# Kernel tuning notes

Hardware: AMD Instinct MI355X
Metric: run time of the kernel (lower is better)

The kernel has to match this reference:

```python
import jax, jax.numpy as jnp
import numpy as np

N = 50000          # nodes in homogeneous graph
E_RAND = 450000    # non-self edges
R = 5              # 4 relations + identity
C = 2              # num_channels
L = 2              # num_layers
IN_DIM = 256
HID = 128
NUM_CLASS = 16
N_CAT = 10000


def setup_inputs() -> dict:
    key = jax.random.key(0)
    ks = jax.random.split(key, 10)
    h = jax.random.normal(ks[0], (N, IN_DIM), dtype=jnp.float32)
    src_r = jax.random.randint(ks[1], (E_RAND,), 0, N, dtype=jnp.int32)
    dst_r = jax.random.randint(ks[2], (E_RAND,), 0, N, dtype=jnp.int32)
    et_r = jax.random.randint(ks[3], (E_RAND,), 0, R - 1, dtype=jnp.int32)
    self_idx = jnp.arange(N, dtype=jnp.int32)
    src = jnp.concatenate([src_r, self_idx])
    dst = jnp.concatenate([dst_r, self_idx])
    etype = jnp.concatenate([et_r, jnp.full((N,), R - 1, dtype=jnp.int32)])
    category_idx = jax.random.randint(ks[4], (N_CAT,), 0, N, dtype=jnp.int32)
    # learned params
    gt_w = 0.01 * jax.random.normal(ks[5], (L, C, R), dtype=jnp.float32)
    Wc = jax.random.normal(ks[6], (C, IN_DIM, HID), dtype=jnp.float32) / np.sqrt(IN_DIM)
    W1 = jax.random.normal(ks[7], (C * HID, HID), dtype=jnp.float32) / np.sqrt(C * HID)
    b1 = jnp.zeros((HID,), dtype=jnp.float32)
    W2 = jax.random.normal(ks[8], (HID, NUM_CLASS), dtype=jnp.float32) / np.sqrt(HID)
    b2 = jnp.zeros((NUM_CLASS,), dtype=jnp.float32)
    return {"h": h, "src": src, "dst": dst, "etype": etype,
            "category_idx": category_idx, "gt_w": gt_w, "Wc": Wc,
            "W1": W1, "b1": b1, "W2": W2, "b2": b2}


def reference(h, src, dst, etype, category_idx, gt_w, Wc, W1, b1, W2, b2):
    n = h.shape[0]
    # per-channel input projection: H[c] = h @ Wc[c]  -> [C, N, HID]
    H = jnp.einsum('nd,cdh->cnh', h, Wc)
    seg = lambda v: jax.ops.segment_sum(v, dst, num_segments=n)
    for l in range(gt_w.shape[0]):
        # GTConv: per-channel softmax over relations; summed weighted adjacency
        Filt = jax.nn.softmax(gt_w[l], axis=1)        # [C, R]
        w = Filt[:, etype]                            # [C, E] edge weights
        # EdgeWeightNorm('right'): divide by weighted in-degree of dst
        deg = jax.vmap(seg)(w)                        # [C, N]
        wn = w / deg[:, dst]                          # [C, E]
        # GCNConv: sum_{e: dst=v} H[src(e)] * wn(e)
        msg = H[:, src, :] * wn[:, :, None]           # [C, E, HID]
        H = jax.vmap(seg)(msg)                        # [C, N, HID]
    # concat channels along feature dim (torch.cat(H, dim=1))
    X = jnp.transpose(H, (1, 0, 2)).reshape(n, -1)    # [N, C*HID]
    X = jax.nn.relu(X @ W1 + b1)
    y = X @ W2 + b2
    return y[category_idx]
```

## Files before the change

### kernel.cpp

```cpp
#include <hip/hip_runtime.h>
#include <hip/hip_bf16.h>

#define IN_DIM 256
#define HID 128
#define CCH 2
#define RR 5
#define LL 2
#define NCLS 16

typedef __attribute__((ext_vector_type(8))) short short8;
typedef __attribute__((ext_vector_type(4))) short short4_;
typedef __attribute__((ext_vector_type(4))) float floatx4;

__device__ __forceinline__ unsigned short f2bf(float f) {
    unsigned int u = __float_as_uint(f);
    unsigned int r = (u + 0x7FFFu + ((u >> 16) & 1u)) >> 16;
    return (unsigned short)r;
}

__global__ void cvt_weights(const float* __restrict__ Wc, const float* __restrict__ W1,
                            const float* __restrict__ gt_w,
                            unsigned short* __restrict__ WcT, unsigned short* __restrict__ W1T,
                            float* __restrict__ filt) {
    int i = blockIdx.x * 256 + threadIdx.x;
    if (blockIdx.x == 0 && threadIdx.x < LL * CCH) {
        const float* g = gt_w + threadIdx.x * RR;
        float m = -1e30f;
        for (int r = 0; r < RR; ++r) m = fmaxf(m, g[r]);
        float e[RR], s = 0.f;
        for (int r = 0; r < RR; ++r) { e[r] = __expf(g[r] - m); s += e[r]; }
        for (int r = 0; r < RR; ++r) filt[threadIdx.x * RR + r] = e[r] / s;
    }
    if (i < CCH * HID * IN_DIM) {
        int c = i >> 15;
        int rem = i & 32767;
        int d = rem >> 8;
        int k = rem & 255;
        WcT[i] = f2bf(Wc[((size_t)c * IN_DIM + k) * HID + d]);
    }
    if (i < HID * IN_DIM) {
        int d = i >> 8;
        int k = i & 255;
        W1T[i] = f2bf(W1[(size_t)k * HID + d]);
    }
}

__global__ __launch_bounds__(256) void proj_mfma(const float* __restrict__ h,
                                                 const unsigned short* __restrict__ WcT,
                                                 unsigned short* __restrict__ H0, int N) {
    int t = threadIdx.x;
    int wv = t >> 6, l = t & 63;
    int l15 = l & 15, lq = l >> 4;
    int node = blockIdx.x * 64 + wv * 16 + l15;
    int nclamp = node < N ? node : N - 1;

    short8 bfrag[8];
    const float* hrow = h + (size_t)nclamp * IN_DIM;
#pragma unroll
    for (int kk = 0; kk < 8; ++kk) {
        int k0 = kk * 32 + lq * 8;
        floatx4 f0 = *(const floatx4*)(hrow + k0);
        floatx4 f1 = *(const floatx4*)(hrow + k0 + 4);
        short8 b;
        b[0] = (short)f2bf(f0[0]); b[1] = (short)f2bf(f0[1]);
        b[2] = (short)f2bf(f0[2]); b[3] = (short)f2bf(f0[3]);
        b[4] = (short)f2bf(f1[0]); b[5] = (short)f2bf(f1[1]);
        b[6] = (short)f2bf(f1[2]); b[7] = (short)f2bf(f1[3]);
        bfrag[kk] = b;
    }

#pragma unroll
    for (int mt = 0; mt < 16; ++mt) {
        floatx4 acc = {0.f, 0.f, 0.f, 0.f};
        const unsigned short* arow = WcT + (size_t)(mt * 16 + l15) * IN_DIM;
#pragma unroll
        for (int kk = 0; kk < 8; ++kk) {
            short8 a = *(const short8*)(arow + kk * 32 + lq * 8);
            acc = __builtin_amdgcn_mfma_f32_16x16x32_bf16(a, bfrag[kk], acc, 0, 0, 0);
        }
        if (node < N) {
            int m0 = mt * 16 + lq * 4;
            short4_ st;
            st[0] = (short)f2bf(acc[0]); st[1] = (short)f2bf(acc[1]);
            st[2] = (short)f2bf(acc[2]); st[3] = (short)f2bf(acc[3]);
            *(short4_*)(H0 + (size_t)node * (CCH * HID) + m0) = st;
        }
    }
}

__global__ void count_kernel(const int* __restrict__ dst, int* __restrict__ counts, int E) {
    for (int e = blockIdx.x * blockDim.x + threadIdx.x; e < E; e += gridDim.x * blockDim.x)
        atomicAdd(&counts[dst[e]], 1);
}

__global__ void scanA_kernel(const int* __restrict__ counts, int* __restrict__ partials, int n) {
    __shared__ int s[256];
    int t = threadIdx.x;
    int i = blockIdx.x * 256 + t;
    int v = (i < n) ? counts[i] : 0;
    s[t] = v;
    __syncthreads();
    for (int off = 1; off < 256; off <<= 1) {
        int tv = (t >= off) ? s[t - off] : 0;
        __syncthreads();
        s[t] += tv;
        __syncthreads();
    }
    if (t == 255) partials[blockIdx.x] = s[255];
}

__global__ void scanB_kernel(const int* __restrict__ partials, int* __restrict__ chunk_off, int nchunk) {
    __shared__ int s[256];
    int t = threadIdx.x;
    int v = (t < nchunk) ? partials[t] : 0;
    s[t] = v;
    __syncthreads();
    for (int off = 1; off < 256; off <<= 1) {
        int tv = (t >= off) ? s[t - off] : 0;
        __syncthreads();
        s[t] += tv;
        __syncthreads();
    }
    if (t < nchunk) chunk_off[t] = s[t] - v;
}

__global__ void scanC_kernel(const int* __restrict__ counts, const int* __restrict__ chunk_off,
                             int* __restrict__ offsets, int* __restrict__ cursor, int n) {
    __shared__ int s[256];
    int t = threadIdx.x;
    int i = blockIdx.x * 256 + t;
    int v = (i < n) ? counts[i] : 0;
    s[t] = v;
    __syncthreads();
    for (int off = 1; off < 256; off <<= 1) {
        int tv = (t >= off) ? s[t - off] : 0;
        __syncthreads();
        s[t] += tv;
        __syncthreads();
    }
    if (i < n) {
        int incl = chunk_off[blockIdx.x] + s[t];
        offsets[i + 1] = incl;
        cursor[i] = incl - v;
    }
    if (i == 0) offsets[0] = 0;
}

__global__ void fill_kernel(const int* __restrict__ src, const int* __restrict__ dst,
                            const int* __restrict__ etype, int* __restrict__ cursor,
                            int2* __restrict__ epack, int E) {
    for (int e = blockIdx.x * blockDim.x + threadIdx.x; e < E; e += gridDim.x * blockDim.x) {
        int d = dst[e];
        int p = atomicAdd(&cursor[d], 1);
        epack[p] = make_int2(src[e], etype[e]);
    }
}

__global__ __launch_bounds__(256) void agg_kernel(const uint4* __restrict__ Hin,
                                                  uint4* __restrict__ Hout,
                                                  const int* __restrict__ offs,
                                                  const int2* __restrict__ epack,
                                                  const float* __restrict__ filt, int N) {
    int node = blockIdx.x;
    int t = threadIdx.x;
    int g = t >> 5;
    int lane32 = t & 31;
    int c = lane32 >> 4;
    float f0 = filt[c * RR + 0], f1 = filt[c * RR + 1], f2 = filt[c * RR + 2];
    float f3 = filt[c * RR + 3], f4 = filt[c * RR + 4];

    int e0 = offs[node], e1 = offs[node + 1];
    float acc[8];
#pragma unroll
    for (int r = 0; r < 8; ++r) acc[r] = 0.f;
    float deg = 0.f;

    for (int j = e0 + g; j < e1; j += 8) {
        int2 pc = epack[j];
        uint4 v = Hin[(size_t)pc.x * 32 + lane32];
        int et = pc.y;
        float w = (et == 0) ? f0 : (et == 1) ? f1 : (et == 2) ? f2 : (et == 3) ? f3 : f4;
        deg += w;
        acc[0] += w * __uint_as_float(v.x << 16);
        acc[1] += w * __uint_as_float(v.x & 0xFFFF0000u);
        acc[2] += w * __uint_as_float(v.y << 16);
        acc[3] += w * __uint_as_float(v.y & 0xFFFF0000u);
        acc[4] += w * __uint_as_float(v.z << 16);
        acc[5] += w * __uint_as_float(v.z & 0xFFFF0000u);
        acc[6] += w * __uint_as_float(v.w << 16);
        acc[7] += w * __uint_as_float(v.w & 0xFFFF0000u);
    }

#pragma unroll
    for (int r = 0; r < 8; ++r) acc[r] += __shfl_xor(acc[r], 32);
    deg += __shfl_xor(deg, 32);

    __shared__ float sacc[3][8][33];
    __shared__ float sdeg[3][33];
    int wv = t >> 6;
    bool lowhalf = (t & 63) < 32;
    if (wv > 0 && lowhalf) {
#pragma unroll
        for (int r = 0; r < 8; ++r) sacc[wv - 1][r][lane32] = acc[r];
        sdeg[wv - 1][lane32] = deg;
    }
    __syncthreads();
    if (wv == 0 && lowhalf) {
#pragma unroll
        for (int k = 0; k < 3; ++k) {
#pragma unroll
            for (int r = 0; r < 8; ++r) acc[r] += sacc[k][r][lane32];
            deg += sdeg[k][lane32];
        }
        float inv = 1.f / deg;
        uint4 o;
        o.x = (unsigned int)f2bf(acc[0] * inv) | ((unsigned int)f2bf(acc[1] * inv) << 16);
        o.y = (unsigned int)f2bf(acc[2] * inv) | ((unsigned int)f2bf(acc[3] * inv) << 16);
        o.z = (unsigned int)f2bf(acc[4] * inv) | ((unsigned int)f2bf(acc[5] * inv) << 16);
        o.w = (unsigned int)f2bf(acc[6] * inv) | ((unsigned int)f2bf(acc[7] * inv) << 16);
        Hout[(size_t)node * 32 + lane32] = o;
    }
}

__global__ __launch_bounds__(256) void mlp1_mfma(const unsigned short* __restrict__ H2,
                                                 const int* __restrict__ cat,
                                                 const unsigned short* __restrict__ W1T,
                                                 const float* __restrict__ b1,
                                                 float* __restrict__ hidden, int NCAT) {
    int t = threadIdx.x;
    int wv = t >> 6, l = t & 63;
    int l15 = l & 15, lq = l >> 4;
    int i = blockIdx.x * 64 + wv * 16 + l15;
    int iclamp = i < NCAT ? i : NCAT - 1;
    int node = cat[iclamp];

    short8 bfrag[8];
    const unsigned short* xrow = H2 + (size_t)node * (CCH * HID);
#pragma unroll
    for (int kk = 0; kk < 8; ++kk)
        bfrag[kk] = *(const short8*)(xrow + kk * 32 + lq * 8);

#pragma unroll
    for (int mt = 0; mt < 8; ++mt) {
        floatx4 acc = {0.f, 0.f, 0.f, 0.f};
        const unsigned short* arow = W1T + (size_t)(mt * 16 + l15) * (CCH * HID);
#pragma unroll
        for (int kk = 0; kk < 8; ++kk) {
            short8 a = *(const short8*)(arow + kk * 32 + lq * 8);
            acc = __builtin_amdgcn_mfma_f32_16x16x32_bf16(a, bfrag[kk], acc, 0, 0, 0);
        }
        if (i < NCAT) {
            int d0 = mt * 16 + lq * 4;
            floatx4 o;
#pragma unroll
            for (int r = 0; r < 4; ++r) o[r] = fmaxf(acc[r] + b1[d0 + r], 0.f);
            *(floatx4*)(hidden + (size_t)i * HID + d0) = o;
        }
    }
}

__global__ void mlp2_kernel(const float* __restrict__ hidden, const float* __restrict__ W2,
                            const float* __restrict__ b2, float* __restrict__ out, int NCAT) {
    int idx = blockIdx.x * 256 + threadIdx.x;
    int i = idx >> 4, cls = idx & 15;
    if (i >= NCAT) return;
    const float* hrow = hidden + (size_t)i * HID;
    float acc = b2[cls];
#pragma unroll 8
    for (int j = 0; j < HID; ++j) acc += hrow[j] * W2[j * NCLS + cls];
    out[idx] = acc;
}

extern "C" void kernel_launch(void* const* d_in, const int* in_sizes, int n_in,
                              void* d_out, int out_size, void* d_ws, size_t ws_size,
                              hipStream_t stream) {
    const float* h    = (const float*)d_in[0];
    const int* src    = (const int*)d_in[1];
    const int* dst    = (const int*)d_in[2];
    const int* etype  = (const int*)d_in[3];
    const int* cat    = (const int*)d_in[4];
    const float* gt_w = (const float*)d_in[5];
    const float* Wc   = (const float*)d_in[6];
    const float* W1   = (const float*)d_in[7];
    const float* b1   = (const float*)d_in[8];
    const float* W2   = (const float*)d_in[9];
    const float* b2   = (const float*)d_in[10];
    float* out = (float*)d_out;

    const int N = in_sizes[0] / IN_DIM;
    const int E = in_sizes[1];
    const int NCAT = in_sizes[4];
    const int NCHUNK = (N + 255) / 256;

    char* p = (char*)d_ws;
    auto alloc = [&](size_t bytes) {
        char* q = p;
        p += (bytes + 255) & ~(size_t)255;
        return q;
    };
    unsigned short* HA   = (unsigned short*)alloc((size_t)N * CCH * HID * 2);
    unsigned short* HB   = (unsigned short*)alloc((size_t)N * CCH * HID * 2);
    unsigned short* WcT  = (unsigned short*)alloc((size_t)CCH * HID * IN_DIM * 2);
    unsigned short* W1T  = (unsigned short*)alloc((size_t)HID * CCH * HID * 2);
    float* hidden        = (float*)alloc((size_t)NCAT * HID * 4);
    int*   counts        = (int*)alloc((size_t)N * 4);
    int*   offsets       = (int*)alloc((size_t)(N + 1) * 4);
    int*   cursor        = (int*)alloc((size_t)N * 4);
    int*   partials      = (int*)alloc((size_t)NCHUNK * 4);
    int*   chunk_off     = (int*)alloc((size_t)NCHUNK * 4);
    int2*  epack         = (int2*)alloc((size_t)E * 8);
    float* filt          = (float*)alloc((size_t)LL * CCH * RR * 4);

    hipMemsetAsync(counts, 0, (size_t)N * 4, stream);

    cvt_weights<<<(CCH * HID * IN_DIM + 255) / 256, 256, 0, stream>>>(Wc, W1, gt_w, WcT, W1T, filt);
    proj_mfma<<<(N + 63) / 64, 256, 0, stream>>>(h, WcT, HA, N);

    count_kernel<<<512, 256, 0, stream>>>(dst, counts, E);
    scanA_kernel<<<NCHUNK, 256, 0, stream>>>(counts, partials, N);
    scanB_kernel<<<1, 256, 0, stream>>>(partials, chunk_off, NCHUNK);
    scanC_kernel<<<NCHUNK, 256, 0, stream>>>(counts, chunk_off, offsets, cursor, N);
    fill_kernel<<<512, 256, 0, stream>>>(src, dst, etype, cursor, epack, E);

    agg_kernel<<<N, 256, 0, stream>>>((const uint4*)HA, (uint4*)HB,
                                      offsets, epack, filt, N);
    agg_kernel<<<N, 256, 0, stream>>>((const uint4*)HB, (uint4*)HA,
                                      offsets, epack, filt + CCH * RR, N);

    mlp1_mfma<<<(NCAT + 63) / 64, 256, 0, stream>>>(HA, cat, W1T, b1, hidden, NCAT);
    mlp2_kernel<<<(NCAT * NCLS + 255) / 256, 256, 0, stream>>>(hidden, W2, b2, out, NCAT);
}
```

Before: 355.7 us.

## Stage node tile in swizzled LDS and split output rows across waves in projection GEMM

The projection kernel now loads the 64-node h tile cooperatively with coalesced float4 reads, converts it to bf16 and stores it in shared memory with an XOR swizzle. Each wave then computes a 64x64 output sub-tile (4x4 MFMA fragments) over all 64 nodes. Before, each wave read all 256 weight rows for its own 16 nodes, so every wave re-fetched the whole weight matrix. The change cuts that weight traffic and improves MFMA reuse, at the cost of 32KB of LDS, a barrier and higher register pressure (launch bounds set to 2 blocks).

```diff
diff --git a/kernel.cpp b/kernel.cpp
--- a/kernel.cpp
+++ b/kernel.cpp
@@ -45,45 +45,80 @@
     }
 }
 
-__global__ __launch_bounds__(256) void proj_mfma(const float* __restrict__ h,
-                                                 const unsigned short* __restrict__ WcT,
-                                                 unsigned short* __restrict__ H0, int N) {
+__global__ __launch_bounds__(256, 2) void proj_mfma(const float* __restrict__ h,
+                                                    const unsigned short* __restrict__ WcT,
+                                                    unsigned short* __restrict__ H0, int N) {
+    __shared__ unsigned short Bl[64 * 256];
     int t = threadIdx.x;
     int wv = t >> 6, l = t & 63;
     int l15 = l & 15, lq = l >> 4;
-    int node = blockIdx.x * 64 + wv * 16 + l15;
-    int nclamp = node < N ? node : N - 1;
-
-    short8 bfrag[8];
-    const float* hrow = h + (size_t)nclamp * IN_DIM;
-#pragma unroll
-    for (int kk = 0; kk < 8; ++kk) {
-        int k0 = kk * 32 + lq * 8;
-        floatx4 f0 = *(const floatx4*)(hrow + k0);
-        floatx4 f1 = *(const floatx4*)(hrow + k0 + 4);
-        short8 b;
-        b[0] = (short)f2bf(f0[0]); b[1] = (short)f2bf(f0[1]);
-        b[2] = (short)f2bf(f0[2]); b[3] = (short)f2bf(f0[3]);
-        b[4] = (short)f2bf(f1[0]); b[5] = (short)f2bf(f1[1]);
-        b[6] = (short)f2bf(f1[2]); b[7] = (short)f2bf(f1[3]);
-        bfrag[kk] = b;
-    }
-
-#pragma unroll
-    for (int mt = 0; mt < 16; ++mt) {
-        floatx4 acc = {0.f, 0.f, 0.f, 0.f};
-        const unsigned short* arow = WcT + (size_t)(mt * 16 + l15) * IN_DIM;
-#pragma unroll
-        for (int kk = 0; kk < 8; ++kk) {
-            short8 a = *(const short8*)(arow + kk * 32 + lq * 8);
-            acc = __builtin_amdgcn_mfma_f32_16x16x32_bf16(a, bfrag[kk], acc, 0, 0, 0);
-        }
-        if (node < N) {
-            int m0 = mt * 16 + lq * 4;
-            short4_ st;
-            st[0] = (short)f2bf(acc[0]); st[1] = (short)f2bf(acc[1]);
-            st[2] = (short)f2bf(acc[2]); st[3] = (short)f2bf(acc[3]);
-            *(short4_*)(H0 + (size_t)node * (CCH * HID) + m0) = st;
+    int n0 = blockIdx.x * 64;
+
+#pragma unroll
+    for (int i = 0; i < 16; ++i) {
+        int fi = t * 4 + i * 1024;
+        int r = fi >> 8;
+        int k = fi & 255;
+        int node = n0 + r;
+        const float* src = h + (size_t)(node < N ? node : N - 1) * IN_DIM + k;
+        floatx4 f = *(const floatx4*)src;
+        short4_ s4;
+        s4[0] = (short)f2bf(f[0]); s4[1] = (short)f2bf(f[1]);
+        s4[2] = (short)f2bf(f[2]); s4[3] = (short)f2bf(f[3]);
+        int c = k >> 3;
+        int half = (k >> 2) & 1;
+        int cs = c ^ ((r & 7) << 2);
+        *(short4_*)(&Bl[r * 256 + cs * 8 + half * 4]) = s4;
+    }
+    __syncthreads();
+
+    floatx4 acc[4][4];
+#pragma unroll
+    for (int m = 0; m < 4; ++m)
+#pragma unroll
+        for (int n = 0; n < 4; ++n) acc[m][n] = (floatx4){0.f, 0.f, 0.f, 0.f};
+
+#pragma unroll
+    for (int kh = 0; kh < 2; ++kh) {
+        short8 a[4][4];
+#pragma unroll
+        for (int mt0 = 0; mt0 < 4; ++mt0) {
+            const unsigned short* arow = WcT + (size_t)((wv * 4 + mt0) * 16 + l15) * IN_DIM;
+#pragma unroll
+            for (int kk = 0; kk < 4; ++kk)
+                a[mt0][kk] = *(const short8*)(arow + (kh * 4 + kk) * 32 + lq * 8);
+        }
+#pragma unroll
+        for (int nf = 0; nf < 4; ++nf) {
+            int r = nf * 16 + l15;
+            short8 b[4];
+#pragma unroll
+            for (int kk = 0; kk < 4; ++kk) {
+                int c = (kh * 4 + kk) * 4 + lq;
+                int cs = c ^ ((r & 7) << 2);
+                b[kk] = *(const short8*)(&Bl[r * 256 + cs * 8]);
+            }
+#pragma unroll
+            for (int mt0 = 0; mt0 < 4; ++mt0)
+#pragma unroll
+                for (int kk = 0; kk < 4; ++kk)
+                    acc[mt0][nf] = __builtin_amdgcn_mfma_f32_16x16x32_bf16(a[mt0][kk], b[kk],
+                                                                           acc[mt0][nf], 0, 0, 0);
+        }
+    }
+
+#pragma unroll
+    for (int mt0 = 0; mt0 < 4; ++mt0) {
+        int m0 = (wv * 4 + mt0) * 16 + lq * 4;
+#pragma unroll
+        for (int nf = 0; nf < 4; ++nf) {
+            int node = n0 + nf * 16 + l15;
+            if (node < N) {
+                short4_ st;
+                st[0] = (short)f2bf(acc[mt0][nf][0]); st[1] = (short)f2bf(acc[mt0][nf][1]);
+                st[2] = (short)f2bf(acc[mt0][nf][2]); st[3] = (short)f2bf(acc[mt0][nf][3]);
+                *(short4_*)(H0 + (size_t)node * (CCH * HID) + m0) = st;
+            }
         }
     }
 }
```

New measurement: 321.1 us. 1.11x faster.
